# Optimization experiments

Measured on AMD Instinct MI355X. Metric: run time of the kernel, lower is better.

## Reference

```python
import jax, jax.numpy as jnp
import numpy as np


def setup_inputs() -> dict:
    key = jax.random.key(0)
    ks = jax.random.split(key, 5)
    B, S, D, F, E = 4, 4096, 512, 2048, 8
    scale = 0.02
    return {
        "x": jax.random.normal(ks[0], (B, S, D), dtype=jnp.float32),
        "gate_w": jax.random.normal(ks[1], (E, D), dtype=jnp.float32) * scale,
        "w1": jax.random.normal(ks[2], (E, F, D), dtype=jnp.float32) * scale,
        "w2": jax.random.normal(ks[3], (E, D, F), dtype=jnp.float32) * scale,
        "w3": jax.random.normal(ks[4], (E, F, D), dtype=jnp.float32) * scale,
        "top_k": 2,
    }


def _moe(x, gate_w, w1, w2, w3, top_k):
    B, S, D = x.shape
    E = gate_w.shape[0]
    xt = x.reshape(-1, D)                       # [T, D], T = B*S
    T = xt.shape[0]

    # --- router: softmax in float32, top-k, renormalize (matches Mixtral) ---
    logits = xt @ gate_w.T                      # [T, E]
    probs = jax.nn.softmax(logits.astype(jnp.float32), axis=-1)
    rw, sel = jax.lax.top_k(probs, top_k)       # [T, k], [T, k]
    rw = rw / jnp.sum(rw, axis=-1, keepdims=True)
    rw = rw.astype(x.dtype)

    # dense combine weights [T, E]: zero for unselected experts
    combine = jnp.zeros((T, E), dtype=x.dtype)
    combine = combine.at[jnp.arange(T)[:, None], sel].add(rw)

    # --- per-expert SwiGLU-style FFN (relu gate), combined by routing weights ---
    out = jnp.zeros_like(xt)
    for e in range(E):  # small fixed expert count
        h = jax.nn.relu(xt @ w1[e].T) * (xt @ w3[e].T)   # [T, F]
        out = out + combine[:, e:e + 1] * (h @ w2[e].T)  # [T, D]
    return out.reshape(B, S, D)


def reference(x, gate_w, w1, w2, w3, top_k):
    return _moe(x, gate_w, w1, w2, w3, top_k)
```

## Files before the change

kernel.cpp:

```cpp
#include <hip/hip_runtime.h>
#include <stdint.h>

#define T_TOK 16384
#define D_DIM 512
#define F_DIM 2048
#define E_NUM 8
#define MAXR  34816

typedef __bf16 bf16x8 __attribute__((ext_vector_type(8)));
typedef float  f32x4  __attribute__((ext_vector_type(4)));

__device__ __forceinline__ unsigned short f2b(float f) {
  union { float f; unsigned u; } a; a.f = f;
  unsigned u = a.u;
  u = u + 0x7fffu + ((u >> 16) & 1u);
  return (unsigned short)(u >> 16);
}
__device__ __forceinline__ float b2f(unsigned short h) {
  union { unsigned u; float f; } a; a.u = ((unsigned)h) << 16;
  return a.f;
}
__device__ __forceinline__ void load_lds16(const void* g, void* l) {
  __builtin_amdgcn_global_load_lds(
      (const __attribute__((address_space(1))) void*)g,
      (__attribute__((address_space(3))) void*)l, 16, 0, 0);
}

#define CSTRIDE 16
#define BAR() __builtin_amdgcn_s_barrier()
#define SP1() __builtin_amdgcn_s_setprio(1)
#define SP0() __builtin_amdgcn_s_setprio(0)
#define VMC6() do { asm volatile("s_waitcnt vmcnt(6)" ::: "memory"); \
                    __builtin_amdgcn_sched_barrier(0); } while (0)
#define VMC2() do { asm volatile("s_waitcnt vmcnt(2)" ::: "memory"); \
                    __builtin_amdgcn_sched_barrier(0); } while (0)

__global__ __launch_bounds__(256) void prelude_kernel(
    const float* __restrict__ x, const float* __restrict__ gw,
    const float* __restrict__ w1, const float* __restrict__ w3,
    const float* __restrict__ w2,
    int* __restrict__ sel, float* __restrict__ rw, unsigned short* __restrict__ xb,
    unsigned short* __restrict__ w1b, unsigned short* __restrict__ w3b,
    unsigned short* __restrict__ w2b)
{
  int b = blockIdx.x;
  if (b < 24576) {
    int seg = b >> 13;
    int i = (b & 8191) * 256 + threadIdx.x;
    const float* s = seg == 0 ? w1 : seg == 1 ? w3 : w2;
    unsigned short* d = seg == 0 ? w1b : seg == 1 ? w3b : w2b;
    float4 v = ((const float4*)s)[i];
    ushort4 o;
    o.x = f2b(v.x); o.y = f2b(v.y); o.z = f2b(v.z); o.w = f2b(v.w);
    ((ushort4*)d)[i] = o;
    return;
  }
  int lane = threadIdx.x & 63;
  int wid  = threadIdx.x >> 6;
  int t = (b - 24576) * 4 + wid;
  const float4* xp = (const float4*)(x + (size_t)t * D_DIM + lane * 8);
  float4 a0 = xp[0], a1 = xp[1];
  ushort4 o0, o1;
  o0.x = f2b(a0.x); o0.y = f2b(a0.y); o0.z = f2b(a0.z); o0.w = f2b(a0.w);
  o1.x = f2b(a1.x); o1.y = f2b(a1.y); o1.z = f2b(a1.z); o1.w = f2b(a1.w);
  ushort4* xbp = (ushort4*)(xb + (size_t)t * D_DIM + lane * 8);
  xbp[0] = o0; xbp[1] = o1;

  float lg[E_NUM];
#pragma unroll
  for (int e = 0; e < E_NUM; ++e) {
    const float4* gp = (const float4*)(gw + (size_t)e * D_DIM + lane * 8);
    float4 g0 = gp[0], g1 = gp[1];
    float s = a0.x*g0.x + a0.y*g0.y + a0.z*g0.z + a0.w*g0.w
            + a1.x*g1.x + a1.y*g1.y + a1.z*g1.z + a1.w*g1.w;
#pragma unroll
    for (int off = 32; off; off >>= 1) s += __shfl_xor(s, off);
    lg[e] = s;
  }
  if (lane == 0) {
    int i0 = 0; float m0 = lg[0];
#pragma unroll
    for (int e = 1; e < E_NUM; ++e) if (lg[e] > m0) { m0 = lg[e]; i0 = e; }
    int i1 = -1; float m1 = -1e30f;
#pragma unroll
    for (int e = 0; e < E_NUM; ++e) if (e != i0 && lg[e] > m1) { m1 = lg[e]; i1 = e; }
    float w0 = 1.0f / (1.0f + expf(m1 - m0));
    sel[2*t] = i0; sel[2*t+1] = i1;
    rw[2*t] = w0;  rw[2*t+1] = 1.0f - w0;
  }
}

__global__ __launch_bounds__(256) void hist_kernel(
    const int* __restrict__ sel, int* __restrict__ counts)
{
  __shared__ int h[E_NUM];
  if (threadIdx.x < E_NUM) h[threadIdx.x] = 0;
  __syncthreads();
  int t = blockIdx.x * 256 + threadIdx.x;
  atomicAdd(&h[sel[2*t]], 1);
  atomicAdd(&h[sel[2*t+1]], 1);
  __syncthreads();
  if (threadIdx.x < E_NUM) atomicAdd(&counts[threadIdx.x * CSTRIDE], h[threadIdx.x]);
}

__global__ void scan_kernel(const int* __restrict__ counts, int* __restrict__ offs,
    int* __restrict__ padTot)
{
  if (threadIdx.x != 0 || blockIdx.x != 0) return;
  int o = 0;
  for (int e = 0; e < E_NUM; ++e) {
    offs[e] = o;
    o += (counts[e * CSTRIDE] + 255) & ~255;
  }
  *padTot = o;
}

__global__ __launch_bounds__(256) void padfill_kernel(
    const int* __restrict__ counts, const int* __restrict__ offs,
    int* __restrict__ ptok, float* __restrict__ pw, int* __restrict__ pexp)
{
  int e = blockIdx.x;
  int c = counts[e * CSTRIDE];
  int o = offs[e];
  int padded = (c + 255) & ~255;
  for (int i = c + threadIdx.x; i < padded; i += 256) {
    ptok[o+i] = 0; pw[o+i] = 0.0f; pexp[o+i] = e;
  }
}

__global__ __launch_bounds__(256) void assign_kernel(
    const int* __restrict__ sel, const float* __restrict__ rw,
    const int* __restrict__ offs, int* __restrict__ cursor,
    int* __restrict__ ptok, float* __restrict__ pw, int* __restrict__ pexp,
    int* __restrict__ t2s)
{
  __shared__ int lcnt[E_NUM];
  __shared__ int base[E_NUM];
  if (threadIdx.x < E_NUM) lcnt[threadIdx.x] = 0;
  __syncthreads();
  int t = blockIdx.x * 256 + threadIdx.x;
  int e[2], rank[2];
  float w[2];
#pragma unroll
  for (int k = 0; k < 2; ++k) {
    e[k] = sel[2*t+k];
    w[k] = rw[2*t+k];
    rank[k] = atomicAdd(&lcnt[e[k]], 1);
  }
  __syncthreads();
  if (threadIdx.x < E_NUM)
    base[threadIdx.x] = atomicAdd(&cursor[threadIdx.x * CSTRIDE], lcnt[threadIdx.x]);
  __syncthreads();
#pragma unroll
  for (int k = 0; k < 2; ++k) {
    int slot = offs[e[k]] + base[e[k]] + rank[k];
    ptok[slot] = t; pw[slot] = w[k]; pexp[slot] = e[k];
    t2s[2*t+k] = slot;
  }
}


__device__ __forceinline__ void stageA8(unsigned short* dst, const unsigned short* xb,
    const int* tokr, int kt, int half, int tid, int csw) {
  int k0 = kt * 64;
#pragma unroll
  for (int r = 0; r < 2; ++r) {
    int h = half*2 + r;
    int rl = h*64 + (tid>>3);
    load_lds16(xb + (size_t)tokr[h]*D_DIM + k0 + csw, &dst[rl*64 + (tid&7)*8]);
  }
}
__device__ __forceinline__ void stageB8(unsigned short* dst, const unsigned short* W,
    int f0, int kt, int tid, int csw) {
  int k0 = kt * 64;
#pragma unroll
  for (int r = 0; r < 2; ++r) {
    int rl = r*64 + (tid>>3);
    load_lds16(W + (size_t)(f0+rl)*D_DIM + k0 + csw, &dst[rl*64 + (tid&7)*8]);
  }
}
__device__ __forceinline__ void readA8(bf16x8 (*af)[2], const unsigned short* buf,
    int wm, int lane, int xs, int mlo) {
#pragma unroll
  for (int m = 0; m < 4; ++m)
#pragma unroll
    for (int s = 0; s < 2; ++s)
      af[m][s] = *(const bf16x8*)&buf[(wm*128 + (mlo+m)*16 + (lane&15))*64 + ((s*32 + ((lane>>4)<<3)) ^ xs)];
}
__device__ __forceinline__ void readB8(bf16x8 (*bf)[2], const unsigned short* buf,
    int wn, int lane, int xs) {
#pragma unroll
  for (int n = 0; n < 2; ++n)
#pragma unroll
    for (int s = 0; s < 2; ++s)
      bf[n][s] = *(const bf16x8*)&buf[(wn*32 + n*16 + (lane&15))*64 + ((s*32 + ((lane>>4)<<3)) ^ xs)];
}
__device__ __forceinline__ void mfmaq(f32x4 (*acc)[2], const bf16x8 (*af)[2], const bf16x8 (*bf)[2]) {
#pragma unroll
  for (int m = 0; m < 4; ++m)
#pragma unroll
    for (int n = 0; n < 2; ++n)
#pragma unroll
      for (int s = 0; s < 2; ++s)
        acc[m][n] = __builtin_amdgcn_mfma_f32_16x16x32_bf16(af[m][s], bf[n][s], acc[m][n], 0, 0, 0);
}

__global__ __launch_bounds__(512, 2) void ffn_h8_kernel(
    const unsigned short* __restrict__ xb, const unsigned short* __restrict__ w1b,
    const unsigned short* __restrict__ w3b, const int* __restrict__ ptok,
    const int* __restrict__ pexp, const int* __restrict__ padTot,
    unsigned short* __restrict__ H)
{
  __shared__ unsigned short As0[256*64], As1[256*64];
  __shared__ unsigned short B1s0[128*64], B1s1[128*64];
  __shared__ unsigned short B3s0[128*64], B3s1[128*64];
  int tm = blockIdx.x >> 4;
  int tn = blockIdx.x & 15;
  int row0 = tm * 256;
  if (row0 >= *padTot) return;
  int e  = pexp[row0];
  int f0 = tn * 128;
  const unsigned short* W1 = w1b + (size_t)e * F_DIM * D_DIM;
  const unsigned short* W3 = w3b + (size_t)e * F_DIM * D_DIM;
  int tid  = threadIdx.x;
  int lane = tid & 63;
  int wid  = tid >> 6;
  int wm = wid >> 2, wn = wid & 3;
  int xs  = (lane & 7) << 3;
  int csw = ((tid & 7) ^ ((tid >> 3) & 7)) * 8;

  int tokr[4];
#pragma unroll
  for (int h = 0; h < 4; ++h) tokr[h] = ptok[row0 + h*64 + (tid>>3)];

  f32x4 acc1[8][2] = {};
  f32x4 acc3[8][2] = {};
  bf16x8 afL[4][2], afH[4][2], b1f[2][2], b3f[2][2];

  stageB8(B1s0, W1, f0, 0, tid, csw);
  stageA8(As0, xb, tokr, 0, 0, tid, csw);
  stageA8(As0, xb, tokr, 0, 1, tid, csw);
  stageB8(B3s0, W3, f0, 0, tid, csw);
  stageB8(B1s1, W1, f0, 1, tid, csw);
  stageA8(As1, xb, tokr, 1, 0, tid, csw);
  stageA8(As1, xb, tokr, 1, 1, tid, csw);
  VMC6();
  BAR();

  for (int i = 0; i < 4; ++i) {
    int ktB = 2*i + 1;
    int s2 = (2*i + 2 < 8) ? 2*i + 2 : 6;
    int s3 = (2*i + 3 < 8) ? 2*i + 3 : 7;
    readA8(afL, As0, wm, lane, xs, 0);
    readB8(b1f, B1s0, wn, lane, xs);
    stageB8(B3s1, W3, f0, ktB, tid, csw);
    BAR(); mfmaq(&acc1[0], afL, b1f); BAR();
    readA8(afH, As0, wm, lane, xs, 4);
    stageB8(B1s0, W1, f0, s2, tid, csw);
    BAR(); mfmaq(&acc1[4], afH, b1f); BAR();
    readB8(b3f, B3s0, wn, lane, xs);
    stageA8(As0, xb, tokr, s2, 0, tid, csw);
    BAR(); mfmaq(&acc3[0], afL, b3f); BAR();
    stageA8(As0, xb, tokr, s2, 1, tid, csw);
    VMC6();
    BAR(); mfmaq(&acc3[4], afH, b3f); BAR();
    readA8(afL, As1, wm, lane, xs, 0);
    readB8(b1f, B1s1, wn, lane, xs);
    stageB8(B3s0, W3, f0, s2, tid, csw);
    BAR(); mfmaq(&acc1[0], afL, b1f); BAR();
    readA8(afH, As1, wm, lane, xs, 4);
    stageB8(B1s1, W1, f0, s3, tid, csw);
    BAR(); mfmaq(&acc1[4], afH, b1f); BAR();
    readB8(b3f, B3s1, wn, lane, xs);
    stageA8(As1, xb, tokr, s3, 0, tid, csw);
    BAR(); mfmaq(&acc3[0], afL, b3f); BAR();
    stageA8(As1, xb, tokr, s3, 1, tid, csw);
    VMC6();
    BAR(); mfmaq(&acc3[4], afH, b3f); BAR();
  }

#pragma unroll
  for (int mi = 0; mi < 8; ++mi) {
    int rbase = row0 + wm*128 + mi*16 + (lane>>4)*4;
#pragma unroll
    for (int ni = 0; ni < 2; ++ni) {
      int col = f0 + wn*32 + ni*16 + (lane & 15);
#pragma unroll
      for (int j = 0; j < 4; ++j) {
        float h = fmaxf(acc1[mi][ni][j], 0.0f) * acc3[mi][ni][j];
        H[(size_t)(rbase + j) * F_DIM + col] = f2b(h);
      }
    }
  }
}

__device__ __forceinline__ void readA_O(bf16x8 (*af)[2], const unsigned short* buf,
    int wm, int lane, int xs) {
#pragma unroll
  for (int m = 0; m < 4; ++m)
#pragma unroll
    for (int s = 0; s < 2; ++s)
      af[m][s] = *(const bf16x8*)&buf[(wm*64 + m*16 + (lane&15))*64 + ((s*32 + ((lane>>4)<<3)) ^ xs)];
}
__device__ __forceinline__ void readB_O(bf16x8* bf, const unsigned short* buf,
    int wn, int lane, int xs) {
#pragma unroll
  for (int s = 0; s < 2; ++s)
    bf[s] = *(const bf16x8*)&buf[(wn*16 + (lane&15))*64 + ((s*32 + ((lane>>4)<<3)) ^ xs)];
}
__device__ __forceinline__ void mfmaO(f32x4* acc, const bf16x8 (*af)[2], const bf16x8* bf) {
  SP1();
#pragma unroll
  for (int m = 0; m < 4; ++m)
#pragma unroll
    for (int s = 0; s < 2; ++s)
      acc[m] = __builtin_amdgcn_mfma_f32_16x16x32_bf16(af[m][s], bf[s], acc[m], 0, 0, 0);
  SP0();
}
__device__ __forceinline__ void stageA_O(unsigned short* dst, const unsigned short* H,
    int row0, int kt, int tid, int csw) {
  int k0 = kt * 64;
#pragma unroll
  for (int r = 0; r < 2; ++r) {
    int rl = r*64 + (tid>>3);
    load_lds16(H + (size_t)(row0+rl)*F_DIM + k0 + csw, &dst[rl*64 + (tid&7)*8]);
  }
}
__device__ __forceinline__ void stageB_O(unsigned short* d1, unsigned short* d3,
    const unsigned short* W2, int d0, int kt, int tid, int csw) {
  int k0 = kt * 64;
  int rl = tid >> 3;
  load_lds16(W2 + (size_t)(d0+rl)*F_DIM + k0 + csw, &d1[rl*64 + (tid&7)*8]);
  load_lds16(W2 + (size_t)(d0+64+rl)*F_DIM + k0 + csw, &d3[rl*64 + (tid&7)*8]);
}

__global__ __launch_bounds__(512, 4) void ffn_out8_kernel(
    const unsigned short* __restrict__ H, const unsigned short* __restrict__ w2b,
    const int* __restrict__ pexp, const float* __restrict__ pw,
    const int* __restrict__ padTot, unsigned short* __restrict__ contrib)
{
  __shared__ unsigned short As0[128*64], As1[128*64];
  __shared__ unsigned short B1s0[64*64], B1s1[64*64];
  __shared__ unsigned short B3s0[64*64], B3s1[64*64];
  int wgid = (blockIdx.x & 7) * 136 + (blockIdx.x >> 3);
  int tm = wgid >> 2;
  int tn = wgid & 3;
  int row0 = tm * 128;
  if (row0 >= *padTot) return;
  int e  = pexp[row0];
  int d0 = tn * 128;
  const unsigned short* W2 = w2b + (size_t)e * D_DIM * F_DIM;
  int tid  = threadIdx.x;
  int lane = tid & 63;
  int wid  = tid >> 6;
  int wm = wid >> 2, wn = wid & 3;
  int xs  = (lane & 7) << 3;
  int csw = ((tid & 7) ^ ((tid >> 3) & 7)) * 8;

  f32x4 acc1[4] = {};
  f32x4 acc3[4] = {};
  bf16x8 af[4][2], b1f[2], b3f[2];

  const int NK = F_DIM / 64;
  stageA_O(As0, H, row0, 0, tid, csw);
  stageB_O(B1s0, B3s0, W2, d0, 0, tid, csw);
  stageA_O(As1, H, row0, 1, tid, csw);
  VMC2();
  BAR();

  for (int i = 0; i < NK/2; ++i) {
    int k1 = 2*i + 1;
    int k2 = (2*i + 2 < NK) ? 2*i + 2 : NK - 1;
    int k3 = (2*i + 3 < NK) ? 2*i + 3 : NK - 1;
    readA_O(af, As0, wm, lane, xs);
    readB_O(b1f, B1s0, wn, lane, xs);
    readB_O(b3f, B3s0, wn, lane, xs);
    stageB_O(B1s1, B3s1, W2, d0, k1, tid, csw);
    BAR(); mfmaO(acc1, af, b1f); BAR();
    stageA_O(As0, H, row0, k2, tid, csw);
    VMC2();
    BAR(); mfmaO(acc3, af, b3f); BAR();
    readA_O(af, As1, wm, lane, xs);
    readB_O(b1f, B1s1, wn, lane, xs);
    readB_O(b3f, B3s1, wn, lane, xs);
    stageB_O(B1s0, B3s0, W2, d0, k2, tid, csw);
    BAR(); mfmaO(acc1, af, b1f); BAR();
    stageA_O(As1, H, row0, k3, tid, csw);
    VMC2();
    BAR(); mfmaO(acc3, af, b3f); BAR();
  }

#pragma unroll
  for (int m = 0; m < 4; ++m) {
    int rbase = row0 + wm*64 + m*16 + (lane>>4)*4;
    float sw[4];
#pragma unroll
    for (int j = 0; j < 4; ++j) sw[j] = pw[rbase + j];
    int colL = d0 + wn*16 + (lane & 15);
#pragma unroll
    for (int j = 0; j < 4; ++j) {
      contrib[(size_t)(rbase + j) * D_DIM + colL]      = f2b(acc1[m][j] * sw[j]);
      contrib[(size_t)(rbase + j) * D_DIM + colL + 64] = f2b(acc3[m][j] * sw[j]);
    }
  }
}

__global__ __launch_bounds__(256) void combine_kernel(
    const unsigned short* __restrict__ contrib, const int* __restrict__ t2s,
    float* __restrict__ out)
{
  int i = blockIdx.x * 256 + threadIdx.x;
  int t = i >> 7;
  int c = (i & 127) * 4;
  int s0 = t2s[2*t], s1 = t2s[2*t+1];
  ushort4 u0 = *(const ushort4*)&contrib[(size_t)s0 * D_DIM + c];
  ushort4 u1 = *(const ushort4*)&contrib[(size_t)s1 * D_DIM + c];
  float4 o;
  o.x = b2f(u0.x) + b2f(u1.x);
  o.y = b2f(u0.y) + b2f(u1.y);
  o.z = b2f(u0.z) + b2f(u1.z);
  o.w = b2f(u0.w) + b2f(u1.w);
  *(float4*)&out[(size_t)t * D_DIM + c] = o;
}

#define OFF_SEL   ((size_t)2048)
#define OFF_RW    (OFF_SEL  + (size_t)2*T_TOK*4)
#define OFF_T2S   (OFF_RW   + (size_t)2*T_TOK*4)
#define OFF_PTOK  (OFF_T2S  + (size_t)2*T_TOK*4)
#define OFF_PW    (OFF_PTOK + (size_t)MAXR*4)
#define OFF_PEXP  (OFF_PW   + (size_t)MAXR*4)
#define OFF_XB    (OFF_PEXP + (size_t)MAXR*4)
#define OFF_W1B   (OFF_XB   + (size_t)T_TOK*D_DIM*2)
#define OFF_W3B   (OFF_W1B  + (size_t)E_NUM*F_DIM*D_DIM*2)
#define OFF_W2B   (OFF_W3B  + (size_t)E_NUM*F_DIM*D_DIM*2)
#define OFF_H     (OFF_W2B  + (size_t)E_NUM*F_DIM*D_DIM*2)
#define OFF_CONTR OFF_XB

extern "C" void kernel_launch(void* const* d_in, const int* in_sizes, int n_in,
                              void* d_out, int out_size, void* d_ws, size_t ws_size,
                              hipStream_t stream) {
  const float* x  = (const float*)d_in[0];
  const float* gw = (const float*)d_in[1];
  const float* w1 = (const float*)d_in[2];
  const float* w2 = (const float*)d_in[3];
  const float* w3 = (const float*)d_in[4];
  float* out = (float*)d_out;
  char* ws = (char*)d_ws;

  int*   counts = (int*)(ws + 0);
  int*   cursor = (int*)(ws + 512);
  int*   offs   = (int*)(ws + 1024);
  int*   padTot = (int*)(ws + 1056);
  int*   sel    = (int*)(ws + OFF_SEL);
  float* rw     = (float*)(ws + OFF_RW);
  int*   t2s    = (int*)(ws + OFF_T2S);
  int*   ptok   = (int*)(ws + OFF_PTOK);
  float* pw     = (float*)(ws + OFF_PW);
  int*   pexp   = (int*)(ws + OFF_PEXP);
  unsigned short* xb      = (unsigned short*)(ws + OFF_XB);
  unsigned short* w1b     = (unsigned short*)(ws + OFF_W1B);
  unsigned short* w3b     = (unsigned short*)(ws + OFF_W3B);
  unsigned short* w2b     = (unsigned short*)(ws + OFF_W2B);
  unsigned short* Hbuf    = (unsigned short*)(ws + OFF_H);
  unsigned short* contrib = (unsigned short*)(ws + OFF_CONTR);

  hipMemsetAsync(ws, 0, 2048, stream);

  prelude_kernel<<<24576 + T_TOK/4, 256, 0, stream>>>(x, gw, w1, w3, w2,
                                                      sel, rw, xb, w1b, w3b, w2b);
  hist_kernel<<<T_TOK/256, 256, 0, stream>>>(sel, counts);
  scan_kernel<<<1, 64, 0, stream>>>(counts, offs, padTot);
  padfill_kernel<<<E_NUM, 256, 0, stream>>>(counts, offs, ptok, pw, pexp);
  assign_kernel<<<T_TOK/256, 256, 0, stream>>>(sel, rw, offs, cursor, ptok, pw, pexp, t2s);

  ffn_h8_kernel<<<(MAXR/256)*(F_DIM/128), 512, 0, stream>>>(xb, w1b, w3b, ptok, pexp, padTot, Hbuf);
  ffn_out8_kernel<<<(MAXR/128)*(D_DIM/128), 512, 0, stream>>>(Hbuf, w2b, pexp, pw, padTot, contrib);
  combine_kernel<<<(T_TOK*D_DIM/4)/256, 256, 0, stream>>>(contrib, t2s, out);

  (void)in_sizes; (void)n_in; (void)out_size; (void)ws_size;
}
```

Before: 316.0 us.

## Run FFN gate/up kernel with 1024 threads and merge scan with pad-fill

The gate/up GEMM kernel now runs 16 waves per 256x128 tile instead of 8, so each wave owns a 64-row slice and half the accumulators. The pipeline is restructured around that, with fewer staged loads per thread, explicit LDS waits, and vmcnt(2) waits. This lowers register pressure and adds waves to hide latency, at the cost of one block per CU and more barriers. Separately, the single-thread scan and the pad-fill kernel are fused into one kernel, removing a launch.

```diff
diff --git a/kernel.cpp b/kernel.cpp
--- a/kernel.cpp
+++ b/kernel.cpp
@@ -30,10 +30,10 @@
 #define BAR() __builtin_amdgcn_s_barrier()
 #define SP1() __builtin_amdgcn_s_setprio(1)
 #define SP0() __builtin_amdgcn_s_setprio(0)
-#define VMC6() do { asm volatile("s_waitcnt vmcnt(6)" ::: "memory"); \
-                    __builtin_amdgcn_sched_barrier(0); } while (0)
 #define VMC2() do { asm volatile("s_waitcnt vmcnt(2)" ::: "memory"); \
                     __builtin_amdgcn_sched_barrier(0); } while (0)
+#define LGKM0() do { asm volatile("s_waitcnt lgkmcnt(0)" ::: "memory"); \
+                     __builtin_amdgcn_sched_barrier(0); } while (0)
 
 __global__ __launch_bounds__(256) void prelude_kernel(
     const float* __restrict__ x, const float* __restrict__ gw,
@@ -103,27 +103,25 @@
   if (threadIdx.x < E_NUM) atomicAdd(&counts[threadIdx.x * CSTRIDE], h[threadIdx.x]);
 }
 
-__global__ void scan_kernel(const int* __restrict__ counts, int* __restrict__ offs,
-    int* __restrict__ padTot)
-{
-  if (threadIdx.x != 0 || blockIdx.x != 0) return;
-  int o = 0;
-  for (int e = 0; e < E_NUM; ++e) {
+__global__ __launch_bounds__(256) void scanpad_kernel(
+    const int* __restrict__ counts, int* __restrict__ offs, int* __restrict__ padTot,
+    int* __restrict__ ptok, float* __restrict__ pw, int* __restrict__ pexp)
+{
+  int e = blockIdx.x;
+  int o = 0, c_e = 0, tot = 0;
+  for (int k = 0; k < E_NUM; ++k) {
+    int c = counts[k * CSTRIDE];
+    int padded = (c + 255) & ~255;
+    if (k < e) o += padded;
+    if (k == e) c_e = c;
+    tot += padded;
+  }
+  if (threadIdx.x == 0) {
     offs[e] = o;
-    o += (counts[e * CSTRIDE] + 255) & ~255;
-  }
-  *padTot = o;
-}
-
-__global__ __launch_bounds__(256) void padfill_kernel(
-    const int* __restrict__ counts, const int* __restrict__ offs,
-    int* __restrict__ ptok, float* __restrict__ pw, int* __restrict__ pexp)
-{
-  int e = blockIdx.x;
-  int c = counts[e * CSTRIDE];
-  int o = offs[e];
-  int padded = (c + 255) & ~255;
-  for (int i = c + threadIdx.x; i < padded; i += 256) {
+    if (e == 0) *padTot = tot;
+  }
+  int padded_e = (c_e + 255) & ~255;
+  for (int i = c_e + threadIdx.x; i < padded_e; i += 256) {
     ptok[o+i] = 0; pw[o+i] = 0.0f; pexp[o+i] = e;
   }
 }
@@ -160,34 +158,30 @@
 }
 
 
-__device__ __forceinline__ void stageA8(unsigned short* dst, const unsigned short* xb,
-    const int* tokr, int kt, int half, int tid, int csw) {
+__device__ __forceinline__ void stageA4(unsigned short* dst, const unsigned short* xb,
+    const int* tokr, int kt, int tid, int csw) {
   int k0 = kt * 64;
 #pragma unroll
-  for (int r = 0; r < 2; ++r) {
-    int h = half*2 + r;
-    int rl = h*64 + (tid>>3);
+  for (int h = 0; h < 2; ++h) {
+    int rl = h*128 + (tid>>3);
     load_lds16(xb + (size_t)tokr[h]*D_DIM + k0 + csw, &dst[rl*64 + (tid&7)*8]);
   }
 }
-__device__ __forceinline__ void stageB8(unsigned short* dst, const unsigned short* W,
+__device__ __forceinline__ void stageB4(unsigned short* d, const unsigned short* W,
     int f0, int kt, int tid, int csw) {
   int k0 = kt * 64;
-#pragma unroll
-  for (int r = 0; r < 2; ++r) {
-    int rl = r*64 + (tid>>3);
-    load_lds16(W + (size_t)(f0+rl)*D_DIM + k0 + csw, &dst[rl*64 + (tid&7)*8]);
-  }
-}
-__device__ __forceinline__ void readA8(bf16x8 (*af)[2], const unsigned short* buf,
-    int wm, int lane, int xs, int mlo) {
+  int rl = tid >> 3;
+  load_lds16(W + (size_t)(f0+rl)*D_DIM + k0 + csw, &d[rl*64 + (tid&7)*8]);
+}
+__device__ __forceinline__ void readA4(bf16x8 (*af)[2], const unsigned short* buf,
+    int wm, int lane, int xs) {
 #pragma unroll
   for (int m = 0; m < 4; ++m)
 #pragma unroll
     for (int s = 0; s < 2; ++s)
-      af[m][s] = *(const bf16x8*)&buf[(wm*128 + (mlo+m)*16 + (lane&15))*64 + ((s*32 + ((lane>>4)<<3)) ^ xs)];
-}
-__device__ __forceinline__ void readB8(bf16x8 (*bf)[2], const unsigned short* buf,
+      af[m][s] = *(const bf16x8*)&buf[(wm*64 + m*16 + (lane&15))*64 + ((s*32 + ((lane>>4)<<3)) ^ xs)];
+}
+__device__ __forceinline__ void readB4(bf16x8 (*bf)[2], const unsigned short* buf,
     int wn, int lane, int xs) {
 #pragma unroll
   for (int n = 0; n < 2; ++n)
@@ -195,7 +189,7 @@
     for (int s = 0; s < 2; ++s)
       bf[n][s] = *(const bf16x8*)&buf[(wn*32 + n*16 + (lane&15))*64 + ((s*32 + ((lane>>4)<<3)) ^ xs)];
 }
-__device__ __forceinline__ void mfmaq(f32x4 (*acc)[2], const bf16x8 (*af)[2], const bf16x8 (*bf)[2]) {
+__device__ __forceinline__ void mfma16(f32x4 (*acc)[2], const bf16x8 (*af)[2], const bf16x8 (*bf)[2]) {
 #pragma unroll
   for (int m = 0; m < 4; ++m)
 #pragma unroll
@@ -205,7 +199,7 @@
         acc[m][n] = __builtin_amdgcn_mfma_f32_16x16x32_bf16(af[m][s], bf[n][s], acc[m][n], 0, 0, 0);
 }
 
-__global__ __launch_bounds__(512, 2) void ffn_h8_kernel(
+__global__ __launch_bounds__(1024) void ffn_h4_kernel(
     const unsigned short* __restrict__ xb, const unsigned short* __restrict__ w1b,
     const unsigned short* __restrict__ w3b, const int* __restrict__ ptok,
     const int* __restrict__ pexp, const int* __restrict__ padTot,
@@ -229,65 +223,62 @@
   int xs  = (lane & 7) << 3;
   int csw = ((tid & 7) ^ ((tid >> 3) & 7)) * 8;
 
-  int tokr[4];
-#pragma unroll
-  for (int h = 0; h < 4; ++h) tokr[h] = ptok[row0 + h*64 + (tid>>3)];
-
-  f32x4 acc1[8][2] = {};
-  f32x4 acc3[8][2] = {};
-  bf16x8 afL[4][2], afH[4][2], b1f[2][2], b3f[2][2];
-
-  stageB8(B1s0, W1, f0, 0, tid, csw);
-  stageA8(As0, xb, tokr, 0, 0, tid, csw);
-  stageA8(As0, xb, tokr, 0, 1, tid, csw);
-  stageB8(B3s0, W3, f0, 0, tid, csw);
-  stageB8(B1s1, W1, f0, 1, tid, csw);
-  stageA8(As1, xb, tokr, 1, 0, tid, csw);
-  stageA8(As1, xb, tokr, 1, 1, tid, csw);
-  VMC6();
+  int tokr[2];
+#pragma unroll
+  for (int h = 0; h < 2; ++h) tokr[h] = ptok[row0 + h*128 + (tid>>3)];
+
+  f32x4 acc1[4][2] = {};
+  f32x4 acc3[4][2] = {};
+  bf16x8 af[4][2], b1f[2][2], b3f[2][2];
+
+  stageA4(As0, xb, tokr, 0, tid, csw);
+  stageB4(B1s0, W1, f0, 0, tid, csw);
+  stageB4(B3s0, W3, f0, 0, tid, csw);
+  stageA4(As1, xb, tokr, 1, tid, csw);
+  VMC2();
   BAR();
 
   for (int i = 0; i < 4; ++i) {
-    int ktB = 2*i + 1;
-    int s2 = (2*i + 2 < 8) ? 2*i + 2 : 6;
-    int s3 = (2*i + 3 < 8) ? 2*i + 3 : 7;
-    readA8(afL, As0, wm, lane, xs, 0);
-    readB8(b1f, B1s0, wn, lane, xs);
-    stageB8(B3s1, W3, f0, ktB, tid, csw);
-    BAR(); mfmaq(&acc1[0], afL, b1f); BAR();
-    readA8(afH, As0, wm, lane, xs, 4);
-    stageB8(B1s0, W1, f0, s2, tid, csw);
-    BAR(); mfmaq(&acc1[4], afH, b1f); BAR();
-    readB8(b3f, B3s0, wn, lane, xs);
-    stageA8(As0, xb, tokr, s2, 0, tid, csw);
-    BAR(); mfmaq(&acc3[0], afL, b3f); BAR();
-    stageA8(As0, xb, tokr, s2, 1, tid, csw);
-    VMC6();
-    BAR(); mfmaq(&acc3[4], afH, b3f); BAR();
-    readA8(afL, As1, wm, lane, xs, 0);
-    readB8(b1f, B1s1, wn, lane, xs);
-    stageB8(B3s0, W3, f0, s2, tid, csw);
-    BAR(); mfmaq(&acc1[0], afL, b1f); BAR();
-    readA8(afH, As1, wm, lane, xs, 4);
-    stageB8(B1s1, W1, f0, s3, tid, csw);
-    BAR(); mfmaq(&acc1[4], afH, b1f); BAR();
-    readB8(b3f, B3s1, wn, lane, xs);
-    stageA8(As1, xb, tokr, s3, 0, tid, csw);
-    BAR(); mfmaq(&acc3[0], afL, b3f); BAR();
-    stageA8(As1, xb, tokr, s3, 1, tid, csw);
-    VMC6();
-    BAR(); mfmaq(&acc3[4], afH, b3f); BAR();
-  }
-
-#pragma unroll
-  for (int mi = 0; mi < 8; ++mi) {
-    int rbase = row0 + wm*128 + mi*16 + (lane>>4)*4;
-#pragma unroll
-    for (int ni = 0; ni < 2; ++ni) {
-      int col = f0 + wn*32 + ni*16 + (lane & 15);
+    int k1 = 2*i + 1;
+    int k2 = (2*i + 2 < 8) ? 2*i + 2 : 7;
+    int k3 = (2*i + 3 < 8) ? 2*i + 3 : 7;
+    readA4(af, As0, wm, lane, xs);
+    readB4(b1f, B1s0, wn, lane, xs);
+    stageB4(B1s1, W1, f0, k1, tid, csw);
+    stageB4(B3s1, W3, f0, k1, tid, csw);
+    BAR(); mfma16(acc1, af, b1f); BAR();
+    readB4(b3f, B3s0, wn, lane, xs);
+    readA4(af, As0, wm, lane, xs);
+    LGKM0();
+    BAR();
+    stageA4(As0, xb, tokr, k2, tid, csw);
+    mfma16(acc3, af, b3f);
+    VMC2();
+    BAR();
+    readA4(af, As1, wm, lane, xs);
+    readB4(b1f, B1s1, wn, lane, xs);
+    stageB4(B1s0, W1, f0, k2, tid, csw);
+    stageB4(B3s0, W3, f0, k2, tid, csw);
+    BAR(); mfma16(acc1, af, b1f); BAR();
+    readB4(b3f, B3s1, wn, lane, xs);
+    readA4(af, As1, wm, lane, xs);
+    LGKM0();
+    BAR();
+    stageA4(As1, xb, tokr, k3, tid, csw);
+    mfma16(acc3, af, b3f);
+    VMC2();
+    BAR();
+  }
+
+#pragma unroll
+  for (int m = 0; m < 4; ++m) {
+    int rbase = row0 + wm*64 + m*16 + (lane>>4)*4;
+#pragma unroll
+    for (int n = 0; n < 2; ++n) {
+      int col = f0 + wn*32 + n*16 + (lane & 15);
 #pragma unroll
       for (int j = 0; j < 4; ++j) {
-        float h = fmaxf(acc1[mi][ni][j], 0.0f) * acc3[mi][ni][j];
+        float h = fmaxf(acc1[m][n][j], 0.0f) * acc3[m][n][j];
         H[(size_t)(rbase + j) * F_DIM + col] = f2b(h);
       }
     }
@@ -469,11 +460,10 @@
   prelude_kernel<<<24576 + T_TOK/4, 256, 0, stream>>>(x, gw, w1, w3, w2,
                                                       sel, rw, xb, w1b, w3b, w2b);
   hist_kernel<<<T_TOK/256, 256, 0, stream>>>(sel, counts);
-  scan_kernel<<<1, 64, 0, stream>>>(counts, offs, padTot);
-  padfill_kernel<<<E_NUM, 256, 0, stream>>>(counts, offs, ptok, pw, pexp);
+  scanpad_kernel<<<E_NUM, 256, 0, stream>>>(counts, offs, padTot, ptok, pw, pexp);
   assign_kernel<<<T_TOK/256, 256, 0, stream>>>(sel, rw, offs, cursor, ptok, pw, pexp, t2s);
 
-  ffn_h8_kernel<<<(MAXR/256)*(F_DIM/128), 512, 0, stream>>>(xb, w1b, w3b, ptok, pexp, padTot, Hbuf);
+  ffn_h4_kernel<<<(MAXR/256)*(F_DIM/128), 1024, 0, stream>>>(xb, w1b, w3b, ptok, pexp, padTot, Hbuf);
   ffn_out8_kernel<<<(MAXR/128)*(D_DIM/128), 512, 0, stream>>>(Hbuf, w2b, pexp, pw, padTot, contrib);
   combine_kernel<<<(T_TOK*D_DIM/4)/256, 256, 0, stream>>>(contrib, t2s, out);
 
```

Measured after the change: 463.6 us. +46.7%, slower.

## Scatter expert outputs via float atomics and merge scan with pad fill

Applied to the files above, without the earlier changes.

The second FFN GEMM now atomically adds its weighted results straight into the zeroed fp32 output, indexed by token. This removes the bf16 contrib buffer, the t2s map and the separate combine kernel. The scan and pad-fill kernels are merged into one launch, with each block recomputing the prefix sum itself. In exchange the output needs a memset, the epilogue issues scattered fp32 atomics, and the summation order becomes nondeterministic. Padding rows point at token 0 with weight 0 and so add zeros to it.

```diff
diff --git a/kernel.cpp b/kernel.cpp
--- a/kernel.cpp
+++ b/kernel.cpp
@@ -15,10 +15,6 @@
   unsigned u = a.u;
   u = u + 0x7fffu + ((u >> 16) & 1u);
   return (unsigned short)(u >> 16);
-}
-__device__ __forceinline__ float b2f(unsigned short h) {
-  union { unsigned u; float f; } a; a.u = ((unsigned)h) << 16;
-  return a.f;
 }
 __device__ __forceinline__ void load_lds16(const void* g, void* l) {
   __builtin_amdgcn_global_load_lds(
@@ -103,27 +99,25 @@
   if (threadIdx.x < E_NUM) atomicAdd(&counts[threadIdx.x * CSTRIDE], h[threadIdx.x]);
 }
 
-__global__ void scan_kernel(const int* __restrict__ counts, int* __restrict__ offs,
-    int* __restrict__ padTot)
-{
-  if (threadIdx.x != 0 || blockIdx.x != 0) return;
-  int o = 0;
-  for (int e = 0; e < E_NUM; ++e) {
+__global__ __launch_bounds__(256) void scanpad_kernel(
+    const int* __restrict__ counts, int* __restrict__ offs, int* __restrict__ padTot,
+    int* __restrict__ ptok, float* __restrict__ pw, int* __restrict__ pexp)
+{
+  int e = blockIdx.x;
+  int o = 0, c_e = 0, tot = 0;
+  for (int k = 0; k < E_NUM; ++k) {
+    int c = counts[k * CSTRIDE];
+    int padded = (c + 255) & ~255;
+    if (k < e) o += padded;
+    if (k == e) c_e = c;
+    tot += padded;
+  }
+  if (threadIdx.x == 0) {
     offs[e] = o;
-    o += (counts[e * CSTRIDE] + 255) & ~255;
-  }
-  *padTot = o;
-}
-
-__global__ __launch_bounds__(256) void padfill_kernel(
-    const int* __restrict__ counts, const int* __restrict__ offs,
-    int* __restrict__ ptok, float* __restrict__ pw, int* __restrict__ pexp)
-{
-  int e = blockIdx.x;
-  int c = counts[e * CSTRIDE];
-  int o = offs[e];
-  int padded = (c + 255) & ~255;
-  for (int i = c + threadIdx.x; i < padded; i += 256) {
+    if (e == 0) *padTot = tot;
+  }
+  int padded_e = (c_e + 255) & ~255;
+  for (int i = c_e + threadIdx.x; i < padded_e; i += 256) {
     ptok[o+i] = 0; pw[o+i] = 0.0f; pexp[o+i] = e;
   }
 }
@@ -131,8 +125,7 @@
 __global__ __launch_bounds__(256) void assign_kernel(
     const int* __restrict__ sel, const float* __restrict__ rw,
     const int* __restrict__ offs, int* __restrict__ cursor,
-    int* __restrict__ ptok, float* __restrict__ pw, int* __restrict__ pexp,
-    int* __restrict__ t2s)
+    int* __restrict__ ptok, float* __restrict__ pw, int* __restrict__ pexp)
 {
   __shared__ int lcnt[E_NUM];
   __shared__ int base[E_NUM];
@@ -155,7 +148,6 @@
   for (int k = 0; k < 2; ++k) {
     int slot = offs[e[k]] + base[e[k]] + rank[k];
     ptok[slot] = t; pw[slot] = w[k]; pexp[slot] = e[k];
-    t2s[2*t+k] = slot;
   }
 }
 
@@ -337,7 +329,8 @@
 __global__ __launch_bounds__(512, 4) void ffn_out8_kernel(
     const unsigned short* __restrict__ H, const unsigned short* __restrict__ w2b,
     const int* __restrict__ pexp, const float* __restrict__ pw,
-    const int* __restrict__ padTot, unsigned short* __restrict__ contrib)
+    const int* __restrict__ ptok, const int* __restrict__ padTot,
+    float* __restrict__ out)
 {
   __shared__ unsigned short As0[128*64], As1[128*64];
   __shared__ unsigned short B1s0[64*64], B1s1[64*64];
@@ -393,40 +386,20 @@
 #pragma unroll
   for (int m = 0; m < 4; ++m) {
     int rbase = row0 + wm*64 + m*16 + (lane>>4)*4;
-    float sw[4];
-#pragma unroll
-    for (int j = 0; j < 4; ++j) sw[j] = pw[rbase + j];
     int colL = d0 + wn*16 + (lane & 15);
 #pragma unroll
     for (int j = 0; j < 4; ++j) {
-      contrib[(size_t)(rbase + j) * D_DIM + colL]      = f2b(acc1[m][j] * sw[j]);
-      contrib[(size_t)(rbase + j) * D_DIM + colL + 64] = f2b(acc3[m][j] * sw[j]);
+      float sw = pw[rbase + j];
+      int   tk = ptok[rbase + j];
+      atomicAdd(&out[(size_t)tk * D_DIM + colL],      acc1[m][j] * sw);
+      atomicAdd(&out[(size_t)tk * D_DIM + colL + 64], acc3[m][j] * sw);
     }
   }
-}
-
-__global__ __launch_bounds__(256) void combine_kernel(
-    const unsigned short* __restrict__ contrib, const int* __restrict__ t2s,
-    float* __restrict__ out)
-{
-  int i = blockIdx.x * 256 + threadIdx.x;
-  int t = i >> 7;
-  int c = (i & 127) * 4;
-  int s0 = t2s[2*t], s1 = t2s[2*t+1];
-  ushort4 u0 = *(const ushort4*)&contrib[(size_t)s0 * D_DIM + c];
-  ushort4 u1 = *(const ushort4*)&contrib[(size_t)s1 * D_DIM + c];
-  float4 o;
-  o.x = b2f(u0.x) + b2f(u1.x);
-  o.y = b2f(u0.y) + b2f(u1.y);
-  o.z = b2f(u0.z) + b2f(u1.z);
-  o.w = b2f(u0.w) + b2f(u1.w);
-  *(float4*)&out[(size_t)t * D_DIM + c] = o;
 }
 
 #define OFF_SEL   ((size_t)2048)
 #define OFF_RW    (OFF_SEL  + (size_t)2*T_TOK*4)
-#define OFF_T2S   (OFF_RW   + (size_t)2*T_TOK*4)
-#define OFF_PTOK  (OFF_T2S  + (size_t)2*T_TOK*4)
+#define OFF_PTOK  (OFF_RW   + (size_t)2*T_TOK*4)
 #define OFF_PW    (OFF_PTOK + (size_t)MAXR*4)
 #define OFF_PEXP  (OFF_PW   + (size_t)MAXR*4)
 #define OFF_XB    (OFF_PEXP + (size_t)MAXR*4)
@@ -434,7 +407,6 @@
 #define OFF_W3B   (OFF_W1B  + (size_t)E_NUM*F_DIM*D_DIM*2)
 #define OFF_W2B   (OFF_W3B  + (size_t)E_NUM*F_DIM*D_DIM*2)
 #define OFF_H     (OFF_W2B  + (size_t)E_NUM*F_DIM*D_DIM*2)
-#define OFF_CONTR OFF_XB
 
 extern "C" void kernel_launch(void* const* d_in, const int* in_sizes, int n_in,
                               void* d_out, int out_size, void* d_ws, size_t ws_size,
@@ -453,7 +425,6 @@
   int*   padTot = (int*)(ws + 1056);
   int*   sel    = (int*)(ws + OFF_SEL);
   float* rw     = (float*)(ws + OFF_RW);
-  int*   t2s    = (int*)(ws + OFF_T2S);
   int*   ptok   = (int*)(ws + OFF_PTOK);
   float* pw     = (float*)(ws + OFF_PW);
   int*   pexp   = (int*)(ws + OFF_PEXP);
@@ -462,20 +433,18 @@
   unsigned short* w3b     = (unsigned short*)(ws + OFF_W3B);
   unsigned short* w2b     = (unsigned short*)(ws + OFF_W2B);
   unsigned short* Hbuf    = (unsigned short*)(ws + OFF_H);
-  unsigned short* contrib = (unsigned short*)(ws + OFF_CONTR);
 
   hipMemsetAsync(ws, 0, 2048, stream);
+  hipMemsetAsync(out, 0, (size_t)T_TOK * D_DIM * 4, stream);
 
   prelude_kernel<<<24576 + T_TOK/4, 256, 0, stream>>>(x, gw, w1, w3, w2,
                                                       sel, rw, xb, w1b, w3b, w2b);
   hist_kernel<<<T_TOK/256, 256, 0, stream>>>(sel, counts);
-  scan_kernel<<<1, 64, 0, stream>>>(counts, offs, padTot);
-  padfill_kernel<<<E_NUM, 256, 0, stream>>>(counts, offs, ptok, pw, pexp);
-  assign_kernel<<<T_TOK/256, 256, 0, stream>>>(sel, rw, offs, cursor, ptok, pw, pexp, t2s);
+  scanpad_kernel<<<E_NUM, 256, 0, stream>>>(counts, offs, padTot, ptok, pw, pexp);
+  assign_kernel<<<T_TOK/256, 256, 0, stream>>>(sel, rw, offs, cursor, ptok, pw, pexp);
 
   ffn_h8_kernel<<<(MAXR/256)*(F_DIM/128), 512, 0, stream>>>(xb, w1b, w3b, ptok, pexp, padTot, Hbuf);
-  ffn_out8_kernel<<<(MAXR/128)*(D_DIM/128), 512, 0, stream>>>(Hbuf, w2b, pexp, pw, padTot, contrib);
-  combine_kernel<<<(T_TOK*D_DIM/4)/256, 256, 0, stream>>>(contrib, t2s, out);
+  ffn_out8_kernel<<<(MAXR/128)*(D_DIM/128), 512, 0, stream>>>(Hbuf, w2b, pexp, pw, ptok, padTot, out);
 
   (void)in_sizes; (void)n_in; (void)out_size; (void)ws_size;
 }
```

After: 395.4 us. 1.25x slower.
